# Kernel tuning notes

Hardware: AMD Instinct MI355X
Metric: run time of the kernel (lower is better)

## Reference

```python
import jax, jax.numpy as jnp
import numpy as np

TAU = 2.0
V_TH = 1.0
ALPHA = 4.0  # spikingjelly surrogate.Sigmoid default
B, L, T, H = 256, 14, 500, 1000

@jax.custom_vjp
def spike(x):
    return (x >= 0.0).astype(x.dtype)

def _spike_fwd(x):
    return spike(x), x

def _spike_bwd(x, g):
    s = jax.nn.sigmoid(ALPHA * x)
    return (g * ALPHA * s * (1.0 - s),)

spike.defvjp(_spike_fwd, _spike_bwd)

def _abs_linear_init(key, out_f, in_f):
    b = 1.0 / np.sqrt(in_f)
    return jnp.abs(jax.random.uniform(key, (out_f, in_f), minval=-b, maxval=b, dtype=jnp.float32))

def setup_inputs() -> dict:
    key = jax.random.key(0)
    ks = jax.random.split(key, 7)
    x = jax.random.normal(ks[0], (B, L, T), dtype=jnp.float32)
    W1 = _abs_linear_init(ks[1], H, L)
    R1 = _abs_linear_init(ks[2], H, H)
    W2 = _abs_linear_init(ks[3], H, H)
    R2 = _abs_linear_init(ks[4], H, H)
    W3 = _abs_linear_init(ks[5], H, H)
    R3 = _abs_linear_init(ks[6], H, H)
    return {"x": x, "W1": W1, "R1": R1, "W2": W2, "R2": R2, "W3": W3, "R3": R3}

def _lif(v, inp):
    # decay_input=True: v += (inp - (v - v_reset)) / tau, v_reset=0, hard reset
    v = v + (inp - v) / TAU
    s = spike(v - V_TH)
    v = v * (1.0 - s)  # hard reset to 0 where spiked
    return v, s

def reference(x, W1, R1, W2, R2, W3, R3):
    bsz = x.shape[0]
    xt = jnp.transpose(x, (2, 0, 1))  # [T, B, L]
    z = jnp.zeros((bsz, H), dtype=x.dtype)
    carry0 = (z, z, z, z, z, z)  # c1,c2,c3 (spike caches), v1,v2,v3 (membranes)

    def step(carry, inp_t):
        c1, c2, c3, v1, v2, v3 = carry
        h1 = inp_t @ W1.T + c1 @ R1.T
        v1, s1 = _lif(v1, h1)
        h2 = s1 @ W2.T + c2 @ R2.T
        v2, s2 = _lif(v2, h2)
        h3 = s2 @ W3.T + c3 @ R3.T
        v3, s3 = _lif(v3, h3)
        return (s1, s2, s3, v1, v2, v3), None

    (c1, c2, c3, v1, v2, v3), _ = jax.lax.scan(step, carry0, xt)
    return jnp.exp(v3)
```

## Files before the change

### kernel.cpp

```cpp
#include <hip/hip_runtime.h>

constexpr int Bsz = 256, Lf = 14, Tt = 500, Hn = 1000;
constexpr int HP = 1024, KP = 1024;
constexpr int NG = 8, GBLK = 32;
constexpr int NBLK = 256;

constexpr size_t W_MAT    = (size_t)HP * KP * 2;
constexpr size_t W_SH     = (size_t)HP * KP;
constexpr size_t SB_OFF   = 5 * W_MAT;
constexpr size_t SB_BYTES = (size_t)2 * 3 * NG * GBLK * KP;
constexpr size_t BAR_OFF  = SB_OFF + SB_BYTES;
constexpr size_t BAR_BYTES = 16384;


typedef __attribute__((ext_vector_type(8)))  short    short8;
typedef __attribute__((ext_vector_type(16))) float    f32x16;
typedef __attribute__((ext_vector_type(4)))  unsigned u32x4v;

__device__ __forceinline__ unsigned short f2bf(float f) {
  unsigned u = __builtin_bit_cast(unsigned, f);
  unsigned r = (u + 0x7FFFu + ((u >> 16) & 1u)) >> 16;
  return (unsigned short)r;
}

__global__ void prep_w(const float* __restrict__ R1, const float* __restrict__ W2,
                       const float* __restrict__ R2, const float* __restrict__ W3,
                       const float* __restrict__ R3, unsigned char* __restrict__ ws) {
  int id  = blockIdx.x * 256 + threadIdx.x;
  int mat = id >> 20;
  int rem = id & 0xFFFFF;
  int h   = rem >> 10;
  int k   = rem & 1023;
  const float* src = (mat == 0) ? R1 : (mat == 1) ? W2 : (mat == 2) ? R2
                    : (mat == 3) ? W3 : R3;
  float v = (h < Hn && k < Hn) ? src[(size_t)h * Hn + k] : 0.f;
  ((unsigned short*)ws)[(size_t)mat * W_SH + (size_t)h * KP + k] = f2bf(v);
}

__device__ __forceinline__ f32x16 MF(short8 a, const unsigned short* wp, f32x16 c) {
  short8 b = *(const short8*)wp;
  return __builtin_amdgcn_mfma_f32_32x32x16_bf16(a, b, c, 0, 0, 0);
}

__device__ __forceinline__ short8 expandBits(unsigned bt) {
  unsigned r0 = (bt & 1u)        * 0x3F80u + (bt & 2u)        * 0x1FC00000u;
  unsigned r1 = ((bt >> 2) & 1u) * 0x3F80u + ((bt >> 2) & 2u) * 0x1FC00000u;
  unsigned r2 = ((bt >> 4) & 1u) * 0x3F80u + ((bt >> 4) & 2u) * 0x1FC00000u;
  unsigned r3 = ((bt >> 6) & 1u) * 0x3F80u + ((bt >> 6) & 2u) * 0x1FC00000u;
  u32x4v u = {r0, r1, r2, r3};
  return __builtin_bit_cast(short8, u);
}

__device__ __forceinline__ unsigned bsel8(const u32x4v q[8], int kc, unsigned shl) {
  unsigned d = q[kc >> 3][(kc >> 1) & 3];
  return (d >> (((kc & 1) << 4) + shl)) & 0xFFu;
}

__device__ __forceinline__ void ldplane(const unsigned char* p, u32x4v q[8]) {
  asm volatile(
    "global_load_dwordx4 %0, %8, off sc0 sc1\n\t"
    "global_load_dwordx4 %1, %8, off offset:16 sc0 sc1\n\t"
    "global_load_dwordx4 %2, %8, off offset:32 sc0 sc1\n\t"
    "global_load_dwordx4 %3, %8, off offset:48 sc0 sc1\n\t"
    "global_load_dwordx4 %4, %8, off offset:64 sc0 sc1\n\t"
    "global_load_dwordx4 %5, %8, off offset:80 sc0 sc1\n\t"
    "global_load_dwordx4 %6, %8, off offset:96 sc0 sc1\n\t"
    "global_load_dwordx4 %7, %8, off offset:112 sc0 sc1"
    : "=&v"(q[0]), "=&v"(q[1]), "=&v"(q[2]), "=&v"(q[3]),
      "=&v"(q[4]), "=&v"(q[5]), "=&v"(q[6]), "=&v"(q[7])
    : "v"(p) : "memory");
}

__device__ __forceinline__ void bits3(const unsigned char* p0,
    const unsigned char* p1, const unsigned char* p2,
    u32x4v& a0, u32x4v& b0, u32x4v& a1, u32x4v& b1, u32x4v& a2, u32x4v& b2) {
  asm volatile(
    "global_load_dwordx4 %0, %6, off sc0 sc1\n\t"
    "global_load_dwordx4 %1, %6, off offset:16 sc0 sc1\n\t"
    "global_load_dwordx4 %2, %7, off sc0 sc1\n\t"
    "global_load_dwordx4 %3, %7, off offset:16 sc0 sc1\n\t"
    "global_load_dwordx4 %4, %8, off sc0 sc1\n\t"
    "global_load_dwordx4 %5, %8, off offset:16 sc0 sc1\n\t"
    "s_waitcnt vmcnt(0)"
    : "=&v"(a0), "=&v"(b0), "=&v"(a1), "=&v"(b1), "=&v"(a2), "=&v"(b2)
    : "v"(p0), "v"(p1), "v"(p2) : "memory");
}
__device__ __forceinline__ unsigned bsel(const u32x4v& a, const u32x4v& b,
                                         int kc, unsigned shl) {
  unsigned q = (kc < 8) ? a[(unsigned)(kc >> 1)] : b[(unsigned)((kc - 8) >> 1)];
  return (q >> (((kc & 1) << 4) + shl)) & 0xFFu;
}

__device__ __forceinline__ unsigned gate_off(int r, int lb) {
  bool rdP[3] = {false, false, false}, wrP[3] = {false, false, false};
#pragma unroll
  for (int i = 0; i < 3; ++i) {
    const int lay = (r * 3 + i) >> 5;
    if (lay == 0)      { rdP[0] = true; wrP[0] = true; }
    else if (lay == 1) { rdP[0] = true; rdP[1] = true; wrP[1] = true; }
    else               { rdP[1] = true; rdP[2] = true; wrP[2] = true; }
  }
  const bool isP[3] = { lb <= 10, lb >= 10 && lb <= 21, lb >= 21 };
  const bool isC[3] = { lb <= 21, lb >= 10, lb >= 21 };
  bool prod = false, cons = false;
#pragma unroll
  for (int pl = 0; pl < 3; ++pl) {
    prod |= rdP[pl] && isP[pl];
    cons |= wrP[pl] && isC[pl];
  }
  return prod ? 0u : (cons ? 1u : 0x40000000u);
}

__global__ void __launch_bounds__(256, 1)
snn_wave(const float* __restrict__ x, const float* __restrict__ W1,
         unsigned char* __restrict__ ws, float* __restrict__ out)
{
  const int tid = threadIdx.x;
  const int l   = tid & 63;
  const int w   = tid >> 6;
  const int lr  = l & 31;
  const int lg  = l >> 5;
  const int blk = blockIdx.x;
  const int g   = blk >> 5;
  const int r   = blk & 31;
  const int b0  = g * GBLK;
  const unsigned shl = (unsigned)lg * 8u;

  unsigned char* sb  = ws + SB_OFF;
  unsigned*      bar = (unsigned*)(ws + BAR_OFF);
  unsigned*      myflag = bar + ((size_t)g * GBLK + r) * 16;
  unsigned*      lanef  = bar + ((size_t)g * GBLK + (l & 31)) * 16;
  const unsigned short* wb = (const unsigned short*)ws;

  const int ti  = (w < 3) ? w : 0;
  const int rt  = r * 3 + ti;
  const int lay = rt >> 5;
  const int hh  = (rt & 31) * 32;
  const size_t wl = (size_t)(hh + lr) * KP + lg * 8;
  const unsigned short *wA, *wB;
  int plA, plB;
  if (lay == 0)      { wA = wb + 0 * W_SH + wl; wB = wA;              plA = 0; plB = 0; }
  else if (lay == 1) { wA = wb + 1 * W_SH + wl; wB = wb + 2 * W_SH + wl; plA = 0; plB = 1; }
  else               { wA = wb + 3 * W_SH + wl; wB = wb + 4 * W_SH + wl; plA = 1; plB = 2; }

  const unsigned off = gate_off(r, l & 31);

  float w1r[Lf];
#pragma unroll
  for (int t = 0; t < Lf; ++t)
    w1r[t] = ((hh + lr) < Hn) ? W1[(size_t)(hh + lr) * Lf + t] : 0.f;

  f32x16 v;
#pragma unroll
  for (int j = 0; j < 16; ++j) v[j] = 0.f;

#pragma unroll 1
  for (int p = 0; p < Tt + 2; ++p) {
    const int srd = (p + 1) & 1;
    const int swr = p & 1;

    float Freg[16];
    if (w < 3 && lay == 0) {
#pragma unroll
      for (int j = 0; j < 16; ++j) {
        float F = 0.f;
        if (p < Tt) {
          const int row = (j & 3) + 8 * (j >> 2) + 4 * lg;
          const float* xr = x + (size_t)(b0 + row) * (Lf * Tt) + p;
#pragma unroll
          for (int t = 0; t < Lf; ++t)
            F = fmaf(xr[(size_t)t * Tt], w1r[t], F);
        }
        Freg[j] = F;
      }
    }

    if (w == 3 && l < 32) {
      for (;;) {
        unsigned fv;
        asm volatile("global_load_dword %0, %1, off sc0 sc1\n\ts_waitcnt vmcnt(0)"
                     : "=v"(fv) : "v"(lanef) : "memory");
        if (__all(fv + off >= (unsigned)p)) break;
        __builtin_amdgcn_s_sleep(1);
      }
    }
    __syncthreads();

    if (w < 3) {
      const size_t rowoff = (size_t)lr * 128;
      u32x4v qA[8], qB[8];
      ldplane(sb + (((size_t)srd * 3 + plA) * NG + g) * 4096 + rowoff, qA);
      if (lay != 0)
        ldplane(sb + (((size_t)srd * 3 + plB) * NG + g) * 4096 + rowoff, qB);
      asm volatile("s_waitcnt vmcnt(0)" ::: "memory");
      __builtin_amdgcn_sched_barrier(0);

      f32x16 acc;
#pragma unroll
      for (int j = 0; j < 16; ++j) acc[j] = 0.f;
      if (lay == 0) {
#pragma unroll
        for (int kc = 0; kc < 64; ++kc)
          acc = MF(expandBits(bsel8(qA, kc, shl)), wA + kc * 16, acc);
      } else {
#pragma unroll
        for (int kc = 0; kc < 64; ++kc) {
          acc = MF(expandBits(bsel8(qA, kc, shl)), wA + kc * 16, acc);
          acc = MF(expandBits(bsel8(qB, kc, shl)), wB + kc * 16, acc);
        }
      }

      unsigned char* ob = sb + (((size_t)swr * 3 + lay) * NG + g) * 4096 + (hh >> 3);
#pragma unroll
      for (int j = 0; j < 16; ++j) {
        const float hs = acc[j] + ((lay == 0) ? Freg[j] : 0.f);
        const float vn = 0.5f * (v[j] + hs);
        const unsigned c = (vn >= 1.0f) ? 1u : 0u;
        v[j] = c ? 0.f : vn;
        unsigned long long m = __ballot(c != 0u);
        if (l == 0) {
          const int r0 = (j & 3) + 8 * (j >> 2);
          asm volatile("global_store_dword %0, %1, off sc0 sc1"
                       :: "v"(ob + (size_t)r0 * 128), "v"((unsigned)m) : "memory");
          asm volatile("global_store_dword %0, %1, off sc0 sc1"
                       :: "v"(ob + (size_t)(r0 + 4) * 128),
                          "v"((unsigned)(m >> 32)) : "memory");
        }
      }
      asm volatile("s_waitcnt vmcnt(0)" ::: "memory");
    }

    __syncthreads();
    if (tid == 0) {
      asm volatile("global_store_dword %0, %1, off sc0 sc1"
                   :: "v"(myflag), "v"((unsigned)(p + 1)) : "memory");
    }
  }

  if (w < 3 && lay == 2 && (hh + lr) < Hn) {
#pragma unroll
    for (int j = 0; j < 16; ++j) {
      const int row = (j & 3) + 8 * (j >> 2) + 4 * lg;
      out[(size_t)(b0 + row) * Hn + hh + lr] = expf(v[j]);
    }
  }
}

__global__ void __launch_bounds__(256, 1)
snn_pipe(const float* __restrict__ x, const float* __restrict__ W1,
         unsigned char* __restrict__ ws, float* __restrict__ out)
{
  __shared__ float lds[12288];

  const int tid = threadIdx.x;
  const int l   = tid & 63;
  const int w   = tid >> 6;
  const int lr  = l & 31;
  const int lg  = l >> 5;
  const int blk = blockIdx.x;
  const int g   = blk >> 5;
  const int r   = blk & 31;
  const int b0  = g * GBLK;
  const unsigned shl = (unsigned)lg * 8u;

  unsigned char* sb  = ws + SB_OFF;
  unsigned*      bar = (unsigned*)(ws + BAR_OFF);
  unsigned*      myflag = bar + ((size_t)g * GBLK + r) * 16;
  unsigned*      lanef  = bar + ((size_t)g * GBLK + (l & 31)) * 16;
  const unsigned short* wb = (const unsigned short*)ws;

  int lay[3], hh[3];
  const unsigned short *wA[3], *wB[3];
#pragma unroll
  for (int i = 0; i < 3; ++i) {
    const int rt = r * 3 + i;
    lay[i] = rt >> 5;
    hh[i]  = (rt & 31) * 32;
    const size_t wl = (size_t)(hh[i] + lr) * KP + w * 256 + lg * 8;
    if (lay[i] == 0)      { wA[i] = wb + 0 * W_SH + wl; wB[i] = wb + 0 * W_SH + wl; }
    else if (lay[i] == 1) { wA[i] = wb + 1 * W_SH + wl; wB[i] = wb + 2 * W_SH + wl; }
    else                  { wA[i] = wb + 3 * W_SH + wl; wB[i] = wb + 4 * W_SH + wl; }
  }

  const unsigned off = gate_off(r, l & 31);

  f32x16 v[3];
#pragma unroll
  for (int i = 0; i < 3; ++i)
#pragma unroll
    for (int j = 0; j < 16; ++j) v[i][j] = 0.f;

#pragma unroll 1
  for (int p = 0; p < Tt + 2; ++p) {
    const int srd = (p + 1) & 1;
    const int swr = p & 1;

#pragma unroll
    for (int i = 0; i < 3; ++i) {
      if (lay[i] != 0) continue;
      const int fh = tid & 31;
      const int fb = tid >> 5;
      float F0 = 0.f, F1 = 0.f, F2 = 0.f, F3 = 0.f;
      if (p < Tt) {
        const int hrow = hh[i] + fh;
        const float* xq0 = x + (size_t)(b0 + fb)      * (Lf * Tt) + p;
        const float* xq1 = x + (size_t)(b0 + fb + 8)  * (Lf * Tt) + p;
        const float* xq2 = x + (size_t)(b0 + fb + 16) * (Lf * Tt) + p;
        const float* xq3 = x + (size_t)(b0 + fb + 24) * (Lf * Tt) + p;
        const float* w1p = W1 + (size_t)hrow * Lf;
#pragma unroll
        for (int t = 0; t < Lf; ++t) {
          const float wv = (hrow < Hn) ? w1p[t] : 0.f;
          F0 = fmaf(xq0[(size_t)t * Tt], wv, F0);
          F1 = fmaf(xq1[(size_t)t * Tt], wv, F1);
          F2 = fmaf(xq2[(size_t)t * Tt], wv, F2);
          F3 = fmaf(xq3[(size_t)t * Tt], wv, F3);
        }
      }
      float* Fp = &lds[9216 + i * 1024 + fb * 32 + fh];
      Fp[0]       = F0;
      Fp[8 * 32]  = F1;
      Fp[16 * 32] = F2;
      Fp[24 * 32] = F3;
    }

    if (tid < 64) {
      for (;;) {
        unsigned fv;
        asm volatile("global_load_dword %0, %1, off sc0 sc1\n\ts_waitcnt vmcnt(0)"
                     : "=v"(fv) : "v"(lanef) : "memory");
        if (__all(fv + off >= (unsigned)p)) break;
        __builtin_amdgcn_s_sleep(1);
      }
    }
    __syncthreads();

    const size_t lslice = (size_t)lr * 128 + (size_t)w * 32;
    const unsigned char* p0 = sb + (((size_t)srd * 3 + 0) * NG + g) * 4096 + lslice;
    const unsigned char* p1 = sb + (((size_t)srd * 3 + 1) * NG + g) * 4096 + lslice;
    const unsigned char* p2 = sb + (((size_t)srd * 3 + 2) * NG + g) * 4096 + lslice;
    u32x4v qa0, qb0, qa1, qb1, qa2, qb2;
    bits3(p0, p1, p2, qa0, qb0, qa1, qb1, qa2, qb2);
    __builtin_amdgcn_sched_barrier(0);

    f32x16 acc[3];
#pragma unroll
    for (int i = 0; i < 3; ++i) {
#pragma unroll
      for (int j = 0; j < 16; ++j) acc[i][j] = 0.f;
      if (lay[i] == 0) {
#pragma unroll
        for (int kc = 0; kc < 16; ++kc)
          acc[i] = MF(expandBits(bsel(qa0, qb0, kc, shl)), wA[i] + kc * 16, acc[i]);
      } else if (lay[i] == 1) {
#pragma unroll
        for (int kc = 0; kc < 16; ++kc) {
          acc[i] = MF(expandBits(bsel(qa0, qb0, kc, shl)), wA[i] + kc * 16, acc[i]);
          acc[i] = MF(expandBits(bsel(qa1, qb1, kc, shl)), wB[i] + kc * 16, acc[i]);
        }
      } else {
#pragma unroll
        for (int kc = 0; kc < 16; ++kc) {
          acc[i] = MF(expandBits(bsel(qa1, qb1, kc, shl)), wA[i] + kc * 16, acc[i]);
          acc[i] = MF(expandBits(bsel(qa2, qb2, kc, shl)), wB[i] + kc * 16, acc[i]);
        }
      }
    }

    if (w != 0) {
      float* dp = &lds[(w - 1) * 3 * 1024 + l];
#pragma unroll
      for (int i = 0; i < 3; ++i)
#pragma unroll
        for (int j = 0; j < 16; ++j) dp[i * 1024 + j * 64] = acc[i][j];
    }
    __syncthreads();

    if (w == 0) {
#pragma unroll
      for (int i = 0; i < 3; ++i) {
        unsigned char* ob = sb + (((size_t)swr * 3 + lay[i]) * NG + g) * 4096
                            + (hh[i] >> 3);
#pragma unroll
        for (int j = 0; j < 16; ++j) {
          const int row = (j & 3) + 8 * (j >> 2) + 4 * lg;
          float a = acc[i][j];
#pragma unroll
          for (int ww = 0; ww < 3; ++ww)
            a += lds[(ww * 3 + i) * 1024 + j * 64 + l];
          const float F = (lay[i] == 0) ? lds[9216 + i * 1024 + row * 32 + lr] : 0.f;
          const float vn = 0.5f * (v[i][j] + a + F);
          const unsigned c = (vn >= 1.0f) ? 1u : 0u;
          v[i][j] = c ? 0.f : vn;
          unsigned long long m = __ballot(c != 0u);
          if (l == 0) {
            const int r0 = (j & 3) + 8 * (j >> 2);
            asm volatile("global_store_dword %0, %1, off sc0 sc1"
                         :: "v"(ob + (size_t)r0 * 128), "v"((unsigned)m) : "memory");
            asm volatile("global_store_dword %0, %1, off sc0 sc1"
                         :: "v"(ob + (size_t)(r0 + 4) * 128),
                            "v"((unsigned)(m >> 32)) : "memory");
          }
        }
      }
    }

    asm volatile("s_waitcnt vmcnt(0)" ::: "memory");
    __syncthreads();
    if (tid == 0) {
      asm volatile("global_store_dword %0, %1, off sc0 sc1"
                   :: "v"(myflag), "v"((unsigned)(p + 1)) : "memory");
    }
    __syncthreads();
  }

  if (w == 0) {
#pragma unroll
    for (int i = 0; i < 3; ++i) {
      if (lay[i] != 2) continue;
      const int h = hh[i] + lr;
      if (h < Hn) {
#pragma unroll
        for (int j = 0; j < 16; ++j) {
          const int row = (j & 3) + 8 * (j >> 2) + 4 * lg;
          out[(size_t)(b0 + row) * Hn + h] = expf(v[i][j]);
        }
      }
    }
  }
}

extern "C" void kernel_launch(void* const* d_in, const int* in_sizes, int n_in,
                              void* d_out, int out_size, void* d_ws, size_t ws_size,
                              hipStream_t stream) {
  const float* x  = (const float*)d_in[0];
  const float* W1 = (const float*)d_in[1];
  const float* R1 = (const float*)d_in[2];
  const float* W2 = (const float*)d_in[3];
  const float* R2 = (const float*)d_in[4];
  const float* W3 = (const float*)d_in[5];
  const float* R3 = (const float*)d_in[6];
  float* out = (float*)d_out;
  unsigned char* ws = (unsigned char*)d_ws;
  (void)ws_size;

  hipLaunchKernelGGL(prep_w, dim3(20480), dim3(256), 0, stream,
                     R1, W2, R2, W3, R3, ws);
  hipMemsetAsync(ws + SB_OFF, 0, SB_BYTES + BAR_BYTES, stream);

  void* args[] = { (void*)&x, (void*)&W1, (void*)&ws, (void*)&out };

  if (hipLaunchCooperativeKernel((const void*)snn_wave, dim3(NBLK), dim3(256),
                                 args, 0, stream) == hipSuccess)
    return;
  hipLaunchCooperativeKernel((const void*)snn_pipe, dim3(NBLK), dim3(256),
                             args, 0, stream);
}
```

Before: 8.154 ms.

## Add triple-buffered ring kernel that overlaps flag polling with compute

Adds a new cooperative kernel as the primary launch path. It uses a three-slot ring of spike bit buffers instead of two. A dedicated wave polls the producer flags for the next step while the other three waves run the MFMA step. Those compute waves signal completion through an LDS atomic counter, replacing a block-wide barrier before the flag store. This is meant to hide inter-block barrier latency and allow one step of slack between producer and consumer blocks, at the cost of extra spin-wait complexity and a subtler memory-ordering argument. The old pipe kernel is removed and the wave kernel becomes the fallback.

```diff
diff --git a/kernel.cpp b/kernel.cpp
--- a/kernel.cpp
+++ b/kernel.cpp
@@ -71,26 +71,6 @@
     : "v"(p) : "memory");
 }
 
-__device__ __forceinline__ void bits3(const unsigned char* p0,
-    const unsigned char* p1, const unsigned char* p2,
-    u32x4v& a0, u32x4v& b0, u32x4v& a1, u32x4v& b1, u32x4v& a2, u32x4v& b2) {
-  asm volatile(
-    "global_load_dwordx4 %0, %6, off sc0 sc1\n\t"
-    "global_load_dwordx4 %1, %6, off offset:16 sc0 sc1\n\t"
-    "global_load_dwordx4 %2, %7, off sc0 sc1\n\t"
-    "global_load_dwordx4 %3, %7, off offset:16 sc0 sc1\n\t"
-    "global_load_dwordx4 %4, %8, off sc0 sc1\n\t"
-    "global_load_dwordx4 %5, %8, off offset:16 sc0 sc1\n\t"
-    "s_waitcnt vmcnt(0)"
-    : "=&v"(a0), "=&v"(b0), "=&v"(a1), "=&v"(b1), "=&v"(a2), "=&v"(b2)
-    : "v"(p0), "v"(p1), "v"(p2) : "memory");
-}
-__device__ __forceinline__ unsigned bsel(const u32x4v& a, const u32x4v& b,
-                                         int kc, unsigned shl) {
-  unsigned q = (kc < 8) ? a[(unsigned)(kc >> 1)] : b[(unsigned)((kc - 8) >> 1)];
-  return (q >> (((kc & 1) << 4) + shl)) & 0xFFu;
-}
-
 __device__ __forceinline__ unsigned gate_off(int r, int lb) {
   bool rdP[3] = {false, false, false}, wrP[3] = {false, false, false};
 #pragma unroll
@@ -109,6 +89,150 @@
     cons |= wrP[pl] && isC[pl];
   }
   return prod ? 0u : (cons ? 1u : 0x40000000u);
+}
+
+__global__ void __launch_bounds__(256, 1)
+snn_ring(const float* __restrict__ x, const float* __restrict__ W1,
+         unsigned char* __restrict__ ws, float* __restrict__ out)
+{
+  __shared__ unsigned dcnt;
+
+  const int tid = threadIdx.x;
+  const int l   = tid & 63;
+  const int w   = tid >> 6;
+  const int lr  = l & 31;
+  const int lg  = l >> 5;
+  const int blk = blockIdx.x;
+  const int g   = blk >> 5;
+  const int r   = blk & 31;
+  const int b0  = g * GBLK;
+  const unsigned shl = (unsigned)lg * 8u;
+
+  unsigned char* sb  = ws + SB_OFF;
+  unsigned*      bar = (unsigned*)(ws + BAR_OFF);
+  unsigned*      myflag = bar + ((size_t)g * GBLK + r) * 16;
+  unsigned*      lanef  = bar + ((size_t)g * GBLK + (l & 31)) * 16;
+  const unsigned short* wb = (const unsigned short*)ws;
+
+  const int ti  = (w < 3) ? w : 0;
+  const int rt  = r * 3 + ti;
+  const int lay = rt >> 5;
+  const int hh  = (rt & 31) * 32;
+  const size_t wl = (size_t)(hh + lr) * KP + lg * 8;
+  const unsigned short *wA, *wB;
+  int plA, plB;
+  if (lay == 0)      { wA = wb + 0 * W_SH + wl; wB = wA;               plA = 0; plB = 0; }
+  else if (lay == 1) { wA = wb + 1 * W_SH + wl; wB = wb + 2 * W_SH + wl; plA = 0; plB = 1; }
+  else               { wA = wb + 3 * W_SH + wl; wB = wb + 4 * W_SH + wl; plA = 1; plB = 2; }
+
+  const unsigned off = gate_off(r, l & 31);
+
+  float w1r[Lf];
+#pragma unroll
+  for (int t = 0; t < Lf; ++t)
+    w1r[t] = ((hh + lr) < Hn) ? W1[(size_t)(hh + lr) * Lf + t] : 0.f;
+
+  if (tid == 0) dcnt = 0;
+  __syncthreads();
+
+  f32x16 v;
+#pragma unroll
+  for (int j = 0; j < 16; ++j) v[j] = 0.f;
+
+  int sw = 0, sr = 2;
+
+#pragma unroll 1
+  for (int p = 0; p < Tt + 2; ++p) {
+    if (w < 3) {
+      float Freg[16];
+      if (lay == 0) {
+#pragma unroll
+        for (int j = 0; j < 16; ++j) {
+          float F = 0.f;
+          if (p < Tt) {
+            const int row = (j & 3) + 8 * (j >> 2) + 4 * lg;
+            const float* xr = x + (size_t)(b0 + row) * (Lf * Tt) + p;
+#pragma unroll
+            for (int t = 0; t < Lf; ++t)
+              F = fmaf(xr[(size_t)t * Tt], w1r[t], F);
+          }
+          Freg[j] = F;
+        }
+      }
+
+      const size_t rowoff = (size_t)lr * 128;
+      u32x4v qA[8], qB[8];
+      ldplane(sb + (((size_t)sr * 3 + plA) * NG + g) * 4096 + rowoff, qA);
+      if (lay != 0)
+        ldplane(sb + (((size_t)sr * 3 + plB) * NG + g) * 4096 + rowoff, qB);
+      asm volatile("s_waitcnt vmcnt(0)" ::: "memory");
+      __builtin_amdgcn_sched_barrier(0);
+
+      f32x16 acc;
+#pragma unroll
+      for (int j = 0; j < 16; ++j) acc[j] = 0.f;
+      if (lay == 0) {
+#pragma unroll
+        for (int kc = 0; kc < 64; ++kc)
+          acc = MF(expandBits(bsel8(qA, kc, shl)), wA + kc * 16, acc);
+      } else {
+#pragma unroll
+        for (int kc = 0; kc < 64; ++kc) {
+          acc = MF(expandBits(bsel8(qA, kc, shl)), wA + kc * 16, acc);
+          acc = MF(expandBits(bsel8(qB, kc, shl)), wB + kc * 16, acc);
+        }
+      }
+
+      unsigned char* ob = sb + (((size_t)sw * 3 + lay) * NG + g) * 4096 + (hh >> 3);
+#pragma unroll
+      for (int j = 0; j < 16; ++j) {
+        const float hs = acc[j] + ((lay == 0) ? Freg[j] : 0.f);
+        const float vn = 0.5f * (v[j] + hs);
+        const unsigned c = (vn >= 1.0f) ? 1u : 0u;
+        v[j] = c ? 0.f : vn;
+        unsigned long long m = __ballot(c != 0u);
+        if (l == 0) {
+          const int r0 = (j & 3) + 8 * (j >> 2);
+          asm volatile("global_store_dword %0, %1, off sc0 sc1"
+                       :: "v"(ob + (size_t)r0 * 128), "v"((unsigned)m) : "memory");
+          asm volatile("global_store_dword %0, %1, off sc0 sc1"
+                       :: "v"(ob + (size_t)(r0 + 4) * 128),
+                          "v"((unsigned)(m >> 32)) : "memory");
+        }
+      }
+      asm volatile("s_waitcnt vmcnt(0)" ::: "memory");
+
+      if (l == 0)
+        __hip_atomic_fetch_add(&dcnt, 1u, __ATOMIC_RELAXED,
+                               __HIP_MEMORY_SCOPE_WORKGROUP);
+      if (w == 0 && l == 0) {
+        while (__hip_atomic_load(&dcnt, __ATOMIC_RELAXED,
+                                 __HIP_MEMORY_SCOPE_WORKGROUP) < 3u * (unsigned)(p + 1)) {}
+        asm volatile("global_store_dword %0, %1, off sc0 sc1"
+                     :: "v"(myflag), "v"((unsigned)(p + 1)) : "memory");
+      }
+    } else if (l < 32 && p < Tt + 1) {
+      for (;;) {
+        unsigned fv;
+        asm volatile("global_load_dword %0, %1, off sc0 sc1\n\ts_waitcnt vmcnt(0)"
+                     : "=v"(fv) : "v"(lanef) : "memory");
+        if (__all(fv + off >= (unsigned)(p + 1))) break;
+        __builtin_amdgcn_s_sleep(1);
+      }
+    }
+    __syncthreads();
+
+    sw = (sw == 2) ? 0 : sw + 1;
+    sr = (sr == 2) ? 0 : sr + 1;
+  }
+
+  if (w < 3 && lay == 2 && (hh + lr) < Hn) {
+#pragma unroll
+    for (int j = 0; j < 16; ++j) {
+      const int row = (j & 3) + 8 * (j >> 2) + 4 * lg;
+      out[(size_t)(b0 + row) * Hn + hh + lr] = expf(v[j]);
+    }
+  }
 }
 
 __global__ void __launch_bounds__(256, 1)
@@ -139,7 +263,7 @@
   const size_t wl = (size_t)(hh + lr) * KP + lg * 8;
   const unsigned short *wA, *wB;
   int plA, plB;
-  if (lay == 0)      { wA = wb + 0 * W_SH + wl; wB = wA;              plA = 0; plB = 0; }
+  if (lay == 0)      { wA = wb + 0 * W_SH + wl; wB = wA;               plA = 0; plB = 0; }
   else if (lay == 1) { wA = wb + 1 * W_SH + wl; wB = wb + 2 * W_SH + wl; plA = 0; plB = 1; }
   else               { wA = wb + 3 * W_SH + wl; wB = wb + 4 * W_SH + wl; plA = 1; plB = 2; }
 
@@ -246,190 +370,6 @@
   }
 }
 
-__global__ void __launch_bounds__(256, 1)
-snn_pipe(const float* __restrict__ x, const float* __restrict__ W1,
-         unsigned char* __restrict__ ws, float* __restrict__ out)
-{
-  __shared__ float lds[12288];
-
-  const int tid = threadIdx.x;
-  const int l   = tid & 63;
-  const int w   = tid >> 6;
-  const int lr  = l & 31;
-  const int lg  = l >> 5;
-  const int blk = blockIdx.x;
-  const int g   = blk >> 5;
-  const int r   = blk & 31;
-  const int b0  = g * GBLK;
-  const unsigned shl = (unsigned)lg * 8u;
-
-  unsigned char* sb  = ws + SB_OFF;
-  unsigned*      bar = (unsigned*)(ws + BAR_OFF);
-  unsigned*      myflag = bar + ((size_t)g * GBLK + r) * 16;
-  unsigned*      lanef  = bar + ((size_t)g * GBLK + (l & 31)) * 16;
-  const unsigned short* wb = (const unsigned short*)ws;
-
-  int lay[3], hh[3];
-  const unsigned short *wA[3], *wB[3];
-#pragma unroll
-  for (int i = 0; i < 3; ++i) {
-    const int rt = r * 3 + i;
-    lay[i] = rt >> 5;
-    hh[i]  = (rt & 31) * 32;
-    const size_t wl = (size_t)(hh[i] + lr) * KP + w * 256 + lg * 8;
-    if (lay[i] == 0)      { wA[i] = wb + 0 * W_SH + wl; wB[i] = wb + 0 * W_SH + wl; }
-    else if (lay[i] == 1) { wA[i] = wb + 1 * W_SH + wl; wB[i] = wb + 2 * W_SH + wl; }
-    else                  { wA[i] = wb + 3 * W_SH + wl; wB[i] = wb + 4 * W_SH + wl; }
-  }
-
-  const unsigned off = gate_off(r, l & 31);
-
-  f32x16 v[3];
-#pragma unroll
-  for (int i = 0; i < 3; ++i)
-#pragma unroll
-    for (int j = 0; j < 16; ++j) v[i][j] = 0.f;
-
-#pragma unroll 1
-  for (int p = 0; p < Tt + 2; ++p) {
-    const int srd = (p + 1) & 1;
-    const int swr = p & 1;
-
-#pragma unroll
-    for (int i = 0; i < 3; ++i) {
-      if (lay[i] != 0) continue;
-      const int fh = tid & 31;
-      const int fb = tid >> 5;
-      float F0 = 0.f, F1 = 0.f, F2 = 0.f, F3 = 0.f;
-      if (p < Tt) {
-        const int hrow = hh[i] + fh;
-        const float* xq0 = x + (size_t)(b0 + fb)      * (Lf * Tt) + p;
-        const float* xq1 = x + (size_t)(b0 + fb + 8)  * (Lf * Tt) + p;
-        const float* xq2 = x + (size_t)(b0 + fb + 16) * (Lf * Tt) + p;
-        const float* xq3 = x + (size_t)(b0 + fb + 24) * (Lf * Tt) + p;
-        const float* w1p = W1 + (size_t)hrow * Lf;
-#pragma unroll
-        for (int t = 0; t < Lf; ++t) {
-          const float wv = (hrow < Hn) ? w1p[t] : 0.f;
-          F0 = fmaf(xq0[(size_t)t * Tt], wv, F0);
-          F1 = fmaf(xq1[(size_t)t * Tt], wv, F1);
-          F2 = fmaf(xq2[(size_t)t * Tt], wv, F2);
-          F3 = fmaf(xq3[(size_t)t * Tt], wv, F3);
-        }
-      }
-      float* Fp = &lds[9216 + i * 1024 + fb * 32 + fh];
-      Fp[0]       = F0;
-      Fp[8 * 32]  = F1;
-      Fp[16 * 32] = F2;
-      Fp[24 * 32] = F3;
-    }
-
-    if (tid < 64) {
-      for (;;) {
-        unsigned fv;
-        asm volatile("global_load_dword %0, %1, off sc0 sc1\n\ts_waitcnt vmcnt(0)"
-                     : "=v"(fv) : "v"(lanef) : "memory");
-        if (__all(fv + off >= (unsigned)p)) break;
-        __builtin_amdgcn_s_sleep(1);
-      }
-    }
-    __syncthreads();
-
-    const size_t lslice = (size_t)lr * 128 + (size_t)w * 32;
-    const unsigned char* p0 = sb + (((size_t)srd * 3 + 0) * NG + g) * 4096 + lslice;
-    const unsigned char* p1 = sb + (((size_t)srd * 3 + 1) * NG + g) * 4096 + lslice;
-    const unsigned char* p2 = sb + (((size_t)srd * 3 + 2) * NG + g) * 4096 + lslice;
-    u32x4v qa0, qb0, qa1, qb1, qa2, qb2;
-    bits3(p0, p1, p2, qa0, qb0, qa1, qb1, qa2, qb2);
-    __builtin_amdgcn_sched_barrier(0);
-
-    f32x16 acc[3];
-#pragma unroll
-    for (int i = 0; i < 3; ++i) {
-#pragma unroll
-      for (int j = 0; j < 16; ++j) acc[i][j] = 0.f;
-      if (lay[i] == 0) {
-#pragma unroll
-        for (int kc = 0; kc < 16; ++kc)
-          acc[i] = MF(expandBits(bsel(qa0, qb0, kc, shl)), wA[i] + kc * 16, acc[i]);
-      } else if (lay[i] == 1) {
-#pragma unroll
-        for (int kc = 0; kc < 16; ++kc) {
-          acc[i] = MF(expandBits(bsel(qa0, qb0, kc, shl)), wA[i] + kc * 16, acc[i]);
-          acc[i] = MF(expandBits(bsel(qa1, qb1, kc, shl)), wB[i] + kc * 16, acc[i]);
-        }
-      } else {
-#pragma unroll
-        for (int kc = 0; kc < 16; ++kc) {
-          acc[i] = MF(expandBits(bsel(qa1, qb1, kc, shl)), wA[i] + kc * 16, acc[i]);
-          acc[i] = MF(expandBits(bsel(qa2, qb2, kc, shl)), wB[i] + kc * 16, acc[i]);
-        }
-      }
-    }
-
-    if (w != 0) {
-      float* dp = &lds[(w - 1) * 3 * 1024 + l];
-#pragma unroll
-      for (int i = 0; i < 3; ++i)
-#pragma unroll
-        for (int j = 0; j < 16; ++j) dp[i * 1024 + j * 64] = acc[i][j];
-    }
-    __syncthreads();
-
-    if (w == 0) {
-#pragma unroll
-      for (int i = 0; i < 3; ++i) {
-        unsigned char* ob = sb + (((size_t)swr * 3 + lay[i]) * NG + g) * 4096
-                            + (hh[i] >> 3);
-#pragma unroll
-        for (int j = 0; j < 16; ++j) {
-          const int row = (j & 3) + 8 * (j >> 2) + 4 * lg;
-          float a = acc[i][j];
-#pragma unroll
-          for (int ww = 0; ww < 3; ++ww)
-            a += lds[(ww * 3 + i) * 1024 + j * 64 + l];
-          const float F = (lay[i] == 0) ? lds[9216 + i * 1024 + row * 32 + lr] : 0.f;
-          const float vn = 0.5f * (v[i][j] + a + F);
-          const unsigned c = (vn >= 1.0f) ? 1u : 0u;
-          v[i][j] = c ? 0.f : vn;
-          unsigned long long m = __ballot(c != 0u);
-          if (l == 0) {
-            const int r0 = (j & 3) + 8 * (j >> 2);
-            asm volatile("global_store_dword %0, %1, off sc0 sc1"
-                         :: "v"(ob + (size_t)r0 * 128), "v"((unsigned)m) : "memory");
-            asm volatile("global_store_dword %0, %1, off sc0 sc1"
-                         :: "v"(ob + (size_t)(r0 + 4) * 128),
-                            "v"((unsigned)(m >> 32)) : "memory");
-          }
-        }
-      }
-    }
-
-    asm volatile("s_waitcnt vmcnt(0)" ::: "memory");
-    __syncthreads();
-    if (tid == 0) {
-      asm volatile("global_store_dword %0, %1, off sc0 sc1"
-                   :: "v"(myflag), "v"((unsigned)(p + 1)) : "memory");
-    }
-    __syncthreads();
-  }
-
-  if (w == 0) {
-#pragma unroll
-    for (int i = 0; i < 3; ++i) {
-      if (lay[i] != 2) continue;
-      const int h = hh[i] + lr;
-      if (h < Hn) {
-#pragma unroll
-        for (int j = 0; j < 16; ++j) {
-          const int row = (j & 3) + 8 * (j >> 2) + 4 * lg;
-          out[(size_t)(b0 + row) * Hn + h] = expf(v[i][j]);
-        }
-      }
-    }
-  }
-}
-
 extern "C" void kernel_launch(void* const* d_in, const int* in_sizes, int n_in,
                               void* d_out, int out_size, void* d_ws, size_t ws_size,
                               hipStream_t stream) {
@@ -450,9 +390,9 @@
 
   void* args[] = { (void*)&x, (void*)&W1, (void*)&ws, (void*)&out };
 
-  if (hipLaunchCooperativeKernel((const void*)snn_wave, dim3(NBLK), dim3(256),
+  if (hipLaunchCooperativeKernel((const void*)snn_ring, dim3(NBLK), dim3(256),
                                  args, 0, stream) == hipSuccess)
     return;
-  hipLaunchCooperativeKernel((const void*)snn_pipe, dim3(NBLK), dim3(256),
+  hipLaunchCooperativeKernel((const void*)snn_wave, dim3(NBLK), dim3(256),
                              args, 0, stream);
 }
```

New measurement: 8.021 ms. About the same (-1.6%).
